# Kernel optimization log

Hardware: AMD Instinct MI355X
Metric: run time of the kernel (lower is better)

## Reference

```python
import jax, jax.numpy as jnp
import numpy as np

H = 16  # heads

def setup_inputs() -> dict:
    key = jax.random.key(0)
    k1, k2, k3 = jax.random.split(key, 3)
    B, N, D = 2, 2048, 1024
    x = jax.random.normal(k1, (B, N, D), dtype=jnp.float32)
    W1 = jax.random.normal(k2, (D, 3 * D), dtype=jnp.float32) * (1.0 / np.sqrt(D))
    b1 = jnp.zeros((3 * D,), dtype=jnp.float32)
    W2 = jax.random.normal(k3, (D, D), dtype=jnp.float32) * (1.0 / np.sqrt(D))
    b2 = jnp.zeros((D,), dtype=jnp.float32)
    return {"x": x, "W1": W1, "b1": b1, "W2": W2, "b2": b2}

def reference(x, W1, b1, W2, b2):
    B, N, D = x.shape
    Dh = D // H  # head dim
    qkv = x @ W1 + b1                         # [B,N,3D]
    q, k, v = jnp.split(qkv, 3, axis=-1)
    q = q.reshape(B, N, H, Dh).transpose(0, 2, 1, 3)  # [B,H,N,Dh]
    k = k.reshape(B, N, H, Dh).transpose(0, 2, 1, 3)
    v = v.reshape(B, N, H, Dh).transpose(0, 2, 1, 3)
    scale = 1.0 / np.sqrt(Dh)
    w = jnp.einsum('bhnd,bhmd->bhnm', q, k) * scale   # [B,H,N,N]
    w = jax.nn.softmax(w, axis=-1)
    out = jnp.einsum('bhnm,bhmd->bhnd', w, v)         # [B,H,N,Dh]
    out = out.transpose(0, 2, 1, 3).reshape(B, N, D)
    return out @ W2 + b2
```

## Files before the change

kernel.cpp:

```cpp
#include <hip/hip_runtime.h>
#include <hip/hip_bf16.h>
#include <stdint.h>

#define B_   2
#define H_   16
#define N_   2048
#define D_   1024
#define DH   64
#define MTOK 4096

#define LOG2E 1.44269504088896f

typedef __attribute__((ext_vector_type(8)))  short bf16x8;
typedef __attribute__((ext_vector_type(4)))  float f32x4;
typedef __attribute__((ext_vector_type(16))) float f32x16;
typedef __attribute__((ext_vector_type(2)))  unsigned u32x2;
typedef __attribute__((ext_vector_type(4)))  unsigned short us4;

#define VMCNT_ASM(N) asm volatile("s_waitcnt vmcnt(" #N ")" ::: "memory")

static __device__ __forceinline__ unsigned short f2bf(float f) {
    union { float f; unsigned u; } v; v.f = f;
    unsigned r = v.u + 0x7fffu + ((v.u >> 16) & 1u);
    return (unsigned short)(r >> 16);
}

static __device__ __forceinline__ unsigned f2u(float x) {
    union { float f; unsigned u; } v; v.f = x; return v.u;
}
static __device__ __forceinline__ float u2f(unsigned x) {
    union { unsigned u; float f; } v; v.u = x; return v.f;
}

static __device__ __forceinline__ unsigned cvt_pk_bf16(float lo, float hi) {
    unsigned r;
    asm("v_cvt_pk_bf16_f32 %0, %1, %2" : "=v"(r) : "v"(lo), "v"(hi));
    return r;
}

static __device__ __forceinline__ bf16x8 frag_from_u32(unsigned a, unsigned b, unsigned c, unsigned d) {
    union { unsigned u[4]; bf16x8 v; } x;
    x.u[0] = a; x.u[1] = b; x.u[2] = c; x.u[3] = d;
    return x.v;
}

static __device__ __forceinline__ void load_lds16(const void* g, void* l) {
    __builtin_amdgcn_global_load_lds(
        (const __attribute__((address_space(1))) unsigned int*)g,
        (__attribute__((address_space(3))) unsigned int*)l, 16, 0, 0);
}

__global__ __launch_bounds__(256) void k_pre(const float* __restrict__ x,
                                             unsigned short* __restrict__ xb,
                                             const float* __restrict__ W1,
                                             unsigned short* __restrict__ w1t,
                                             const float* __restrict__ W2,
                                             unsigned short* __restrict__ w2t) {
    int blk = blockIdx.x;
    int t = threadIdx.x;
    if (blk < 4096) {
        int idx = (blk * 256 + t) * 4;
        float4 v = *(const float4*)(x + idx);
        us4 o;
        o.x = f2bf(v.x); o.y = f2bf(v.y); o.z = f2bf(v.z); o.w = f2bf(v.w);
        *(us4*)(xb + idx) = o;
        return;
    }
    const float* in;
    unsigned short* out;
    int C, bx, by;
    if (blk < 4864) { in = W1; out = w1t; C = 3072; int b2 = blk - 4096; bx = b2 % 48; by = b2 / 48; }
    else            { in = W2; out = w2t; C = 1024; int b2 = blk - 4864; bx = b2 % 16; by = b2 / 16; }
    const int R = 1024;
    __shared__ float tile[64][65];
    int c0 = bx * 64, r0 = by * 64;
    int tr = t >> 4, tc = (t & 15) * 4;
#pragma unroll
    for (int p = 0; p < 4; p++) {
        int row = p * 16 + tr;
        float4 v = *(const float4*)(in + (size_t)(r0 + row) * C + c0 + tc);
        tile[row][tc + 0] = v.x; tile[row][tc + 1] = v.y;
        tile[row][tc + 2] = v.z; tile[row][tc + 3] = v.w;
    }
    __syncthreads();
    int oc = t >> 4, orr = (t & 15) * 4;
#pragma unroll
    for (int p = 0; p < 4; p++) {
        int crow = p * 16 + oc;
        us4 o;
        o.x = f2bf(tile[orr + 0][crow]);
        o.y = f2bf(tile[orr + 1][crow]);
        o.z = f2bf(tile[orr + 2][crow]);
        o.w = f2bf(tile[orr + 3][crow]);
        *(us4*)(out + (size_t)(c0 + crow) * R + r0 + orr) = o;
    }
}

__global__ __launch_bounds__(512, 2) void k_gemm0(const unsigned short* __restrict__ A,
                                                  const unsigned short* __restrict__ Bt,
                                                  const float* __restrict__ bias,
                                                  unsigned short* __restrict__ qdst,
                                                  unsigned short* __restrict__ kdst,
                                                  unsigned short* __restrict__ vdst) {
    __shared__ unsigned short lds[57344];
    const int K = 1024, NT = 16;
    int tid = threadIdx.x;
    int lane = tid & 63, wv = tid >> 6;
    int wm = wv >> 2, wn = wv & 3;
    int F = blockIdx.x;
    int L = (F & 7) * 32 + (F >> 3);
    int n0 = (L % 16) * 192;
    int m0 = (L / 16) * 256;

    f32x4 acc[8][3];
#pragma unroll
    for (int i = 0; i < 8; i++)
#pragma unroll
        for (int j = 0; j < 3; j++) {
            f32x4 z; z[0] = 0.f; z[1] = 0.f; z[2] = 0.f; z[3] = 0.f;
            acc[i][j] = z;
        }

    auto stage = [&](int t) {
        int p = t & 1;
        int k0 = t * 64;
        unsigned short* ab = &lds[p * 16384];
        unsigned short* bb = &lds[32768 + p * 12288];
#pragma unroll
        for (int i = 0; i < 4; i++) {
            int u = i * 512 + tid;
            int r = u >> 3, c8 = u & 7;
            int c8s = c8 ^ (r & 7);
            int db = (i * 512 + wv * 64) * 8;
            load_lds16(A + (size_t)(m0 + r) * K + k0 + c8s * 8, &ab[db]);
            if (i < 3)
                load_lds16(Bt + (size_t)(n0 + r) * K + k0 + c8s * 8, &bb[db]);
        }
    };

    stage(0);
    stage(1);

    const int ml = lane & 15, ul = lane >> 4;
    bf16x8 afr[4], bfr[3];

#pragma unroll 1
    for (int t = 0; t < NT; ++t) {
        if (t < NT - 1) { VMCNT_ASM(7); }
        else            { VMCNT_ASM(0); }
        __builtin_amdgcn_s_barrier();

        const unsigned short* ab = &lds[(t & 1) * 16384];
        const unsigned short* bb = &lds[32768 + (t & 1) * 12288];

#pragma unroll
        for (int kk = 0; kk < 2; ++kk) {
            int ck = ((kk * 4 + ul) ^ (ml & 7)) * 8;
#pragma unroll
            for (int mh = 0; mh < 2; ++mh) {
                if (mh == 0) {
#pragma unroll
                    for (int nj = 0; nj < 3; nj++)
                        bfr[nj] = *(const bf16x8*)&bb[(wn * 48 + nj * 16 + ml) * 64 + ck];
                }
#pragma unroll
                for (int q = 0; q < 4; q++)
                    afr[q] = *(const bf16x8*)&ab[(wm * 128 + (mh * 4 + q) * 16 + ml) * 64 + ck];
                __builtin_amdgcn_s_barrier();
                __builtin_amdgcn_s_setprio(1);
#pragma unroll
                for (int q = 0; q < 4; q++)
#pragma unroll
                    for (int nj = 0; nj < 3; nj++)
                        acc[mh * 4 + q][nj] = __builtin_amdgcn_mfma_f32_16x16x32_bf16(
                            afr[q], bfr[nj], acc[mh * 4 + q][nj], 0, 0, 0);
                __builtin_amdgcn_s_setprio(0);
                __builtin_amdgcn_s_barrier();
            }
        }
        if (t + 2 < NT) stage(t + 2);
    }

#pragma unroll
    for (int nj = 0; nj < 3; nj++) {
        int col = n0 + wn * 48 + nj * 16 + (lane & 15);
        float bv = bias[col];
        int which = col >> 10;
        int hd = (col >> 6) & 15;
        int dh = col & 63;
        float scl = (which == 0) ? (0.125f * LOG2E) : 1.0f;
#pragma unroll
        for (int mi = 0; mi < 8; mi++) {
            int rbase = m0 + wm * 128 + mi * 16 + (lane >> 4) * 4;
#pragma unroll
            for (int r = 0; r < 4; r++) {
                int tok = rbase + r;
                int bb2 = tok >> 11, nn = tok & 2047;
                float vvv = (acc[mi][nj][r] + bv) * scl;
                size_t chunk = ((size_t)(bb2 * H_ + hd) * 64 + (nn >> 5)) * 2048;
                if (which == 0) {
                    qdst[((size_t)(bb2 * H_ + hd) * N_ + nn) * DH + dh] = f2bf(vvv);
                } else if (which == 1) {
                    int lane2 = ((dh >> 3) & 1) * 32 + (nn & 31);
                    kdst[chunk + (dh >> 4) * 512 + lane2 * 8 + (dh & 7)] = f2bf(vvv);
                } else {
                    int lane2 = ((nn >> 3) & 1) * 32 + (dh & 31);
                    int islot = (dh >> 5) * 2 + ((nn >> 4) & 1);
                    vdst[chunk + islot * 512 + lane2 * 8 + (nn & 7)] = f2bf(vvv);
                }
            }
        }
    }
}

__global__ __launch_bounds__(256) void k_gemm1(const unsigned short* __restrict__ A,
                                               const unsigned short* __restrict__ Bt,
                                               const float* __restrict__ bias,
                                               float* __restrict__ outp) {
    __shared__ unsigned short As[3][128 * 32];
    __shared__ unsigned short Bs[3][128 * 32];
    const int K = 1024;
    const int NT = 32;
    int tid = threadIdx.x;
    int lane = tid & 63, wv = tid >> 6;
    int wm = wv >> 1, wn = wv & 1;

    const int NX = 8, CPX = 32;
    int F = blockIdx.x;
    int L = (F & 7) * CPX + (F >> 3);
    int n0 = (L % NX) * 128;
    int m0 = (L / NX) * 128;
    int bIdx = m0 >> 11;
    int ntok0 = m0 & 2047;

    f32x4 acc[4][4];
#pragma unroll
    for (int i = 0; i < 4; i++)
#pragma unroll
        for (int j = 0; j < 4; j++) {
            f32x4 z; z[0] = 0.f; z[1] = 0.f; z[2] = 0.f; z[3] = 0.f;
            acc[i][j] = z;
        }

    auto stage = [&](int buf, int tt) {
        int k0 = tt * 32;
        int hh = k0 >> 6;
        const unsigned short* aptr = A + ((size_t)(bIdx * H_ + hh) * N_ + ntok0) * DH + (k0 & 63);
        const unsigned short* bptr = Bt + (size_t)n0 * K + k0;
#pragma unroll
        for (int i = 0; i < 2; i++) {
            int cidb = i * 256 + wv * 64;
            int cid = cidb + lane;
            int row = cid >> 2;
            int cg  = (cid & 3) ^ (row & 3);
            load_lds16(aptr + (size_t)row * DH + cg * 8, &As[buf][cidb * 8]);
            load_lds16(bptr + (size_t)row * K  + cg * 8, &Bs[buf][cidb * 8]);
        }
    };

    stage(0, 0);
    stage(1, 1);

    const int swz = ((lane >> 4) ^ (lane & 3)) * 8;
    const int ar0 = (wm * 64 + (lane & 15)) * 32 + swz;
    const int br0 = (wn * 64 + (lane & 15)) * 32 + swz;

#pragma unroll 1
    for (int t = 0; t < NT; ++t) {
        int cur = t % 3;
        if (t <= NT - 3) stage((t + 2) % 3, t + 2);
        if (t <= NT - 3)      { VMCNT_ASM(8); }
        else if (t == NT - 2) { VMCNT_ASM(4); }
        else                  { VMCNT_ASM(0); }
        __builtin_amdgcn_s_barrier();
        __builtin_amdgcn_sched_barrier(0);

        bf16x8 af[4], bfr[4];
#pragma unroll
        for (int mi = 0; mi < 4; mi++)
            af[mi] = *(const bf16x8*)&As[cur][ar0 + mi * 16 * 32];
#pragma unroll
        for (int ni = 0; ni < 4; ni++)
            bfr[ni] = *(const bf16x8*)&Bs[cur][br0 + ni * 16 * 32];
#pragma unroll
        for (int mi = 0; mi < 4; mi++)
#pragma unroll
            for (int ni = 0; ni < 4; ni++)
                acc[mi][ni] = __builtin_amdgcn_mfma_f32_16x16x32_bf16(
                    af[mi], bfr[ni], acc[mi][ni], 0, 0, 0);

        __builtin_amdgcn_s_barrier();
    }

#pragma unroll
    for (int ni = 0; ni < 4; ni++) {
        int col = n0 + wn * 64 + ni * 16 + (lane & 15);
        float bv = bias[col];
#pragma unroll
        for (int mi = 0; mi < 4; mi++) {
            int rbase = m0 + wm * 64 + mi * 16 + (lane >> 4) * 4;
#pragma unroll
            for (int r = 0; r < 4; r++)
                outp[(size_t)(rbase + r) * D_ + col] = acc[mi][ni][r] + bv;
        }
    }
}

__global__ __launch_bounds__(512, 2) void k_attn(const unsigned short* __restrict__ qh,
                                                 const unsigned short* __restrict__ ks,
                                                 const unsigned short* __restrict__ vs,
                                                 unsigned short* __restrict__ o) {
    __shared__ unsigned short smem[32768];
    unsigned short* kb = smem;
    unsigned short* vb = smem + 16384;
    float* red = (float*)smem;

    int tid = threadIdx.x;
    int lane = tid & 63, wv = tid >> 6;
    int qsub = wv >> 1;
    int kvh  = wv & 1;
    int F = blockIdx.x;
    int L = (F & 7) * 64 + (F >> 3);
    int bh = L >> 4;
    int q0 = (L & 15) * 128 + qsub * 32;
    int ln = lane & 31, hi = lane >> 5;
    const size_t bhO = (size_t)bh * N_ * DH;

    const unsigned short* qp = qh + bhO;
    bf16x8 qf[4];
#pragma unroll
    for (int kk = 0; kk < 4; kk++)
        qf[kk] = *(const bf16x8*)(qp + (size_t)(q0 + ln) * DH + kk * 16 + hi * 8);

    const unsigned short* kg = ks + (size_t)bh * 131072;
    const unsigned short* vg = vs + (size_t)bh * 131072;

    int sbuf = wv >> 1;
    int sl   = wv & 1;
    int sh   = sbuf & 1;
    unsigned short* dstb = ((sbuf >> 1) ? vb : kb) + sh * 8192 + sl * 2048;
    const unsigned short* srcb = ((sbuf >> 1) ? vg : kg) + (size_t)sh * 65536 + sl * 2048;
    auto stageT = [&](int ring, int t) {
#pragma unroll
        for (int i = 0; i < 4; i++)
            load_lds16(srcb + (size_t)t * 4096 + i * 512 + lane * 8,
                       dstb + ring * 4096 + i * 512);
    };

    f32x16 o0, o1;
#pragma unroll
    for (int r = 0; r < 16; r++) { o0[r] = 0.f; o1[r] = 0.f; }
    float m = -INFINITY, l = 0.f;

    stageT(0, 0);
    __syncthreads();

#pragma unroll 1
    for (int t = 0; t < 16; ++t) {
        int b = t & 1;
        if (t < 15) stageT(b ^ 1, t + 1);

        const unsigned short* kB = kb + kvh * 8192 + b * 4096;
        const unsigned short* vB = vb + kvh * 8192 + b * 4096;

        bf16x8 kfa[4], kfb[4];
#pragma unroll
        for (int i = 0; i < 4; i++) {
            kfa[i] = *(const bf16x8*)&kB[i * 512 + lane * 8];
            kfb[i] = *(const bf16x8*)&kB[2048 + i * 512 + lane * 8];
        }
        f32x16 sa, sb;
#pragma unroll
        for (int r = 0; r < 16; r++) { sa[r] = 0.f; sb[r] = 0.f; }
        __builtin_amdgcn_s_setprio(1);
#pragma unroll
        for (int i = 0; i < 4; i++)
            sa = __builtin_amdgcn_mfma_f32_32x32x16_bf16(kfa[i], qf[i], sa, 0, 0, 0);
#pragma unroll
        for (int i = 0; i < 4; i++)
            sb = __builtin_amdgcn_mfma_f32_32x32x16_bf16(kfb[i], qf[i], sb, 0, 0, 0);
        __builtin_amdgcn_s_setprio(0);

        float mx[8];
#pragma unroll
        for (int i = 0; i < 8; i++)
            mx[i] = fmaxf(fmaxf(sa[i], sa[i + 8]), fmaxf(sb[i], sb[i + 8]));
#pragma unroll
        for (int i = 0; i < 4; i++) mx[i] = fmaxf(mx[i], mx[i + 4]);
        float mt = fmaxf(fmaxf(mx[0], mx[2]), fmaxf(mx[1], mx[3]));
        {
            u32x2 sw = __builtin_amdgcn_permlane32_swap(f2u(mt), f2u(mt), false, false);
            mt = fmaxf(u2f(sw[0]), u2f(sw[1]));
        }
        if (!__all(mt <= m + 8.0f)) {
            float mn = fmaxf(m, mt);
            float fs = __builtin_amdgcn_exp2f(m - mn);
            m = mn;
            l *= fs;
#pragma unroll
            for (int r = 0; r < 16; r++) { o0[r] *= fs; o1[r] *= fs; }
        }
        float pa[16], pb[16];
#pragma unroll
        for (int r = 0; r < 16; r++) {
            pa[r] = __builtin_amdgcn_exp2f(sa[r] - m);
            pb[r] = __builtin_amdgcn_exp2f(sb[r] - m);
        }
        float sm[8];
#pragma unroll
        for (int i = 0; i < 8; i++) sm[i] = (pa[i] + pa[i + 8]) + (pb[i] + pb[i + 8]);
#pragma unroll
        for (int i = 0; i < 4; i++) sm[i] = sm[i] + sm[i + 4];
        float sum = (sm[0] + sm[2]) + (sm[1] + sm[3]);
        {
            u32x2 sw = __builtin_amdgcn_permlane32_swap(f2u(sum), f2u(sum), false, false);
            sum = u2f(sw[0]) + u2f(sw[1]);
        }
        l += sum;

        unsigned pka[8], pkb[8];
#pragma unroll
        for (int i = 0; i < 8; i++) {
            pka[i] = cvt_pk_bf16(pa[2 * i], pa[2 * i + 1]);
            pkb[i] = cvt_pk_bf16(pb[2 * i], pb[2 * i + 1]);
        }
        u32x2 s0 = __builtin_amdgcn_permlane32_swap(pka[0], pka[2], false, false);
        u32x2 s1 = __builtin_amdgcn_permlane32_swap(pka[1], pka[3], false, false);
        u32x2 s2 = __builtin_amdgcn_permlane32_swap(pka[4], pka[6], false, false);
        u32x2 s3 = __builtin_amdgcn_permlane32_swap(pka[5], pka[7], false, false);
        bf16x8 pf0 = frag_from_u32(s0[0], s1[0], s0[1], s1[1]);
        bf16x8 pf1 = frag_from_u32(s2[0], s3[0], s2[1], s3[1]);
        s0 = __builtin_amdgcn_permlane32_swap(pkb[0], pkb[2], false, false);
        s1 = __builtin_amdgcn_permlane32_swap(pkb[1], pkb[3], false, false);
        s2 = __builtin_amdgcn_permlane32_swap(pkb[4], pkb[6], false, false);
        s3 = __builtin_amdgcn_permlane32_swap(pkb[5], pkb[7], false, false);
        bf16x8 pf2 = frag_from_u32(s0[0], s1[0], s0[1], s1[1]);
        bf16x8 pf3 = frag_from_u32(s2[0], s3[0], s2[1], s3[1]);

        bf16x8 vf0, vf1, vf2, vf3;
        vf0 = *(const bf16x8*)&vB[0 * 512 + lane * 8];
        vf1 = *(const bf16x8*)&vB[1 * 512 + lane * 8];
        vf2 = *(const bf16x8*)&vB[2048 + 0 * 512 + lane * 8];
        vf3 = *(const bf16x8*)&vB[2048 + 1 * 512 + lane * 8];
        __builtin_amdgcn_s_setprio(1);
        o0 = __builtin_amdgcn_mfma_f32_32x32x16_bf16(vf0, pf0, o0, 0, 0, 0);
        o0 = __builtin_amdgcn_mfma_f32_32x32x16_bf16(vf1, pf1, o0, 0, 0, 0);
        o0 = __builtin_amdgcn_mfma_f32_32x32x16_bf16(vf2, pf2, o0, 0, 0, 0);
        o0 = __builtin_amdgcn_mfma_f32_32x32x16_bf16(vf3, pf3, o0, 0, 0, 0);
        __builtin_amdgcn_s_setprio(0);
        vf0 = *(const bf16x8*)&vB[2 * 512 + lane * 8];
        vf1 = *(const bf16x8*)&vB[3 * 512 + lane * 8];
        vf2 = *(const bf16x8*)&vB[2048 + 2 * 512 + lane * 8];
        vf3 = *(const bf16x8*)&vB[2048 + 3 * 512 + lane * 8];
        __builtin_amdgcn_s_setprio(1);
        o1 = __builtin_amdgcn_mfma_f32_32x32x16_bf16(vf0, pf0, o1, 0, 0, 0);
        o1 = __builtin_amdgcn_mfma_f32_32x32x16_bf16(vf1, pf1, o1, 0, 0, 0);
        o1 = __builtin_amdgcn_mfma_f32_32x32x16_bf16(vf2, pf2, o1, 0, 0, 0);
        o1 = __builtin_amdgcn_mfma_f32_32x32x16_bf16(vf3, pf3, o1, 0, 0, 0);
        __builtin_amdgcn_s_setprio(0);

        __syncthreads();
    }

    if (kvh == 1) {
        float* rp = red + (qsub * 64 + lane) * 34;
#pragma unroll
        for (int r = 0; r < 16; r++) { rp[r] = o0[r]; rp[16 + r] = o1[r]; }
        rp[32] = m;
        rp[33] = l;
    }
    __syncthreads();
    if (kvh == 0) {
        const float* rp = red + (qsub * 64 + lane) * 34;
        float mb = rp[32], lb = rp[33];
        float mn = fmaxf(m, mb);
        float fa = __builtin_amdgcn_exp2f(m - mn);
        float fb = __builtin_amdgcn_exp2f(mb - mn);
        float inv = 1.0f / (l * fa + lb * fb);
        float ga = fa * inv, gb = fb * inv;
        unsigned short* ob = o + bhO + (size_t)(q0 + ln) * DH;
#pragma unroll
        for (int t2 = 0; t2 < 2; t2++) {
#pragma unroll
            for (int g = 0; g < 4; g++) {
                int d = t2 * 32 + g * 8 + hi * 4;
                int rb = g * 4;
                float a0 = (t2 ? o1[rb + 0] : o0[rb + 0]) * ga + rp[t2 * 16 + rb + 0] * gb;
                float a1 = (t2 ? o1[rb + 1] : o0[rb + 1]) * ga + rp[t2 * 16 + rb + 1] * gb;
                float a2 = (t2 ? o1[rb + 2] : o0[rb + 2]) * ga + rp[t2 * 16 + rb + 2] * gb;
                float a3 = (t2 ? o1[rb + 3] : o0[rb + 3]) * ga + rp[t2 * 16 + rb + 3] * gb;
                us4 w;
                w.x = f2bf(a0); w.y = f2bf(a1); w.z = f2bf(a2); w.w = f2bf(a3);
                *(us4*)(ob + d) = w;
            }
        }
    }
}

extern "C" void kernel_launch(void* const* d_in, const int* in_sizes, int n_in,
                              void* d_out, int out_size, void* d_ws, size_t ws_size,
                              hipStream_t stream) {
    const float* x  = (const float*)d_in[0];
    const float* W1 = (const float*)d_in[1];
    const float* b1 = (const float*)d_in[2];
    const float* W2 = (const float*)d_in[3];
    const float* b2 = (const float*)d_in[4];
    float* out = (float*)d_out;

    char* ws = (char*)d_ws;
    unsigned short* xb   = (unsigned short*)(ws);
    unsigned short* w1t  = (unsigned short*)(ws + 8388608);
    unsigned short* w2t  = (unsigned short*)(ws + 14680064);
    unsigned short* qh   = (unsigned short*)(ws + 16777216);
    unsigned short* ks   = (unsigned short*)(ws + 25165824);
    unsigned short* vsb  = (unsigned short*)(ws + 33554432);
    unsigned short* attn = (unsigned short*)(ws + 41943040);

    k_pre<<<5120, 256, 0, stream>>>(x, xb, W1, w1t, W2, w2t);
    k_gemm0<<<256, 512, 0, stream>>>(xb, w1t, b1, qh, ks, vsb);
    k_attn<<<512, 512, 0, stream>>>(qh, ks, vsb, attn);
    k_gemm1<<<256, 256, 0, stream>>>(attn, w2t, b2, out);
}
```

Measured before the change: 119.9 us.

## Software-pipeline attention QK^T with previous tile softmax-PV and retile output GEMM

The attention loop is restructured so the QK^T MFMAs for tile t are issued in the same iteration as the softmax and PV of tile t-1. V gets a triple-buffered LDS ring, which grows LDS from 64KB to 80KB. This is meant to overlap softmax VALU work with matrix work, at the cost of more LDS per block and possibly lower occupancy. Separately, the output-projection GEMM moves to 512 threads per block with K-steps of 64 and a double-buffered, XOR-swizzled LDS layout, issuing the next stage after compute instead of keeping a triple-buffer ring.

Result: faster. 110.2 us (-8.1%).

```diff
diff --git a/kernel.cpp b/kernel.cpp
--- a/kernel.cpp
+++ b/kernel.cpp
@@ -213,95 +213,96 @@
     }
 }
 
-__global__ __launch_bounds__(256) void k_gemm1(const unsigned short* __restrict__ A,
-                                               const unsigned short* __restrict__ Bt,
-                                               const float* __restrict__ bias,
-                                               float* __restrict__ outp) {
-    __shared__ unsigned short As[3][128 * 32];
-    __shared__ unsigned short Bs[3][128 * 32];
-    const int K = 1024;
-    const int NT = 32;
+__global__ __launch_bounds__(512, 2) void k_gemm1(const unsigned short* __restrict__ A,
+                                                  const unsigned short* __restrict__ Bt,
+                                                  const float* __restrict__ bias,
+                                                  float* __restrict__ outp) {
+    __shared__ unsigned short lds1[32768];
+    const int K = 1024, NT = 16;
     int tid = threadIdx.x;
     int lane = tid & 63, wv = tid >> 6;
-    int wm = wv >> 1, wn = wv & 1;
-
-    const int NX = 8, CPX = 32;
+    int wm = wv >> 2, wn = wv & 3;
     int F = blockIdx.x;
-    int L = (F & 7) * CPX + (F >> 3);
-    int n0 = (L % NX) * 128;
-    int m0 = (L / NX) * 128;
+    int L = (F & 7) * 32 + (F >> 3);
+    int n0 = (L % 8) * 128;
+    int m0 = (L / 8) * 128;
     int bIdx = m0 >> 11;
     int ntok0 = m0 & 2047;
 
-    f32x4 acc[4][4];
+    f32x4 acc[4][2];
 #pragma unroll
     for (int i = 0; i < 4; i++)
 #pragma unroll
-        for (int j = 0; j < 4; j++) {
+        for (int j = 0; j < 2; j++) {
             f32x4 z; z[0] = 0.f; z[1] = 0.f; z[2] = 0.f; z[3] = 0.f;
             acc[i][j] = z;
         }
 
-    auto stage = [&](int buf, int tt) {
-        int k0 = tt * 32;
-        int hh = k0 >> 6;
-        const unsigned short* aptr = A + ((size_t)(bIdx * H_ + hh) * N_ + ntok0) * DH + (k0 & 63);
-        const unsigned short* bptr = Bt + (size_t)n0 * K + k0;
+    auto stage = [&](int t) {
+        int p = t & 1;
+        const unsigned short* aptr = A + ((size_t)(bIdx * H_ + t) * N_ + ntok0) * DH;
+        const unsigned short* bptr = Bt + (size_t)n0 * K + t * 64;
+        unsigned short* ab = &lds1[p * 8192];
+        unsigned short* bb = &lds1[16384 + p * 8192];
 #pragma unroll
         for (int i = 0; i < 2; i++) {
-            int cidb = i * 256 + wv * 64;
-            int cid = cidb + lane;
-            int row = cid >> 2;
-            int cg  = (cid & 3) ^ (row & 3);
-            load_lds16(aptr + (size_t)row * DH + cg * 8, &As[buf][cidb * 8]);
-            load_lds16(bptr + (size_t)row * K  + cg * 8, &Bs[buf][cidb * 8]);
+            int u = i * 512 + tid;
+            int r = u >> 3, c8 = u & 7;
+            int c8s = c8 ^ (r & 7);
+            int db = (i * 512 + wv * 64) * 8;
+            load_lds16(aptr + (size_t)r * DH + c8s * 8, &ab[db]);
+            load_lds16(bptr + (size_t)r * K  + c8s * 8, &bb[db]);
         }
     };
 
-    stage(0, 0);
-    stage(1, 1);
-
-    const int swz = ((lane >> 4) ^ (lane & 3)) * 8;
-    const int ar0 = (wm * 64 + (lane & 15)) * 32 + swz;
-    const int br0 = (wn * 64 + (lane & 15)) * 32 + swz;
+    stage(0);
+    stage(1);
+
+    const int ml = lane & 15, ul = lane >> 4;
+    bf16x8 afr[4], bfr[2];
 
 #pragma unroll 1
     for (int t = 0; t < NT; ++t) {
-        int cur = t % 3;
-        if (t <= NT - 3) stage((t + 2) % 3, t + 2);
-        if (t <= NT - 3)      { VMCNT_ASM(8); }
-        else if (t == NT - 2) { VMCNT_ASM(4); }
-        else                  { VMCNT_ASM(0); }
+        if (t < NT - 1) { VMCNT_ASM(4); }
+        else            { VMCNT_ASM(0); }
         __builtin_amdgcn_s_barrier();
-        __builtin_amdgcn_sched_barrier(0);
-
-        bf16x8 af[4], bfr[4];
-#pragma unroll
-        for (int mi = 0; mi < 4; mi++)
-            af[mi] = *(const bf16x8*)&As[cur][ar0 + mi * 16 * 32];
-#pragma unroll
-        for (int ni = 0; ni < 4; ni++)
-            bfr[ni] = *(const bf16x8*)&Bs[cur][br0 + ni * 16 * 32];
-#pragma unroll
-        for (int mi = 0; mi < 4; mi++)
-#pragma unroll
-            for (int ni = 0; ni < 4; ni++)
-                acc[mi][ni] = __builtin_amdgcn_mfma_f32_16x16x32_bf16(
-                    af[mi], bfr[ni], acc[mi][ni], 0, 0, 0);
-
-        __builtin_amdgcn_s_barrier();
-    }
-
-#pragma unroll
-    for (int ni = 0; ni < 4; ni++) {
-        int col = n0 + wn * 64 + ni * 16 + (lane & 15);
+
+        const unsigned short* ab = &lds1[(t & 1) * 8192];
+        const unsigned short* bb = &lds1[16384 + (t & 1) * 8192];
+
+#pragma unroll
+        for (int kk = 0; kk < 2; ++kk) {
+            int ck = ((kk * 4 + ul) ^ (ml & 7)) * 8;
+#pragma unroll
+            for (int nj = 0; nj < 2; nj++)
+                bfr[nj] = *(const bf16x8*)&bb[(wn * 32 + nj * 16 + ml) * 64 + ck];
+#pragma unroll
+            for (int q = 0; q < 4; q++)
+                afr[q] = *(const bf16x8*)&ab[(wm * 64 + q * 16 + ml) * 64 + ck];
+            __builtin_amdgcn_s_barrier();
+            __builtin_amdgcn_s_setprio(1);
+#pragma unroll
+            for (int q = 0; q < 4; q++)
+#pragma unroll
+                for (int nj = 0; nj < 2; nj++)
+                    acc[q][nj] = __builtin_amdgcn_mfma_f32_16x16x32_bf16(
+                        afr[q], bfr[nj], acc[q][nj], 0, 0, 0);
+            __builtin_amdgcn_s_setprio(0);
+            __builtin_amdgcn_s_barrier();
+        }
+        if (t + 2 < NT) stage(t + 2);
+    }
+
+#pragma unroll
+    for (int nj = 0; nj < 2; nj++) {
+        int col = n0 + wn * 32 + nj * 16 + ml;
         float bv = bias[col];
 #pragma unroll
         for (int mi = 0; mi < 4; mi++) {
             int rbase = m0 + wm * 64 + mi * 16 + (lane >> 4) * 4;
 #pragma unroll
             for (int r = 0; r < 4; r++)
-                outp[(size_t)(rbase + r) * D_ + col] = acc[mi][ni][r] + bv;
+                outp[(size_t)(rbase + r) * D_ + col] = acc[mi][nj][r] + bv;
         }
     }
 }
@@ -310,7 +311,7 @@
                                                  const unsigned short* __restrict__ ks,
                                                  const unsigned short* __restrict__ vs,
                                                  unsigned short* __restrict__ o) {
-    __shared__ unsigned short smem[32768];
+    __shared__ unsigned short smem[40960];
     unsigned short* kb = smem;
     unsigned short* vb = smem + 16384;
     float* red = (float*)smem;
@@ -338,13 +339,14 @@
     int sbuf = wv >> 1;
     int sl   = wv & 1;
     int sh   = sbuf & 1;
-    unsigned short* dstb = ((sbuf >> 1) ? vb : kb) + sh * 8192 + sl * 2048;
     const unsigned short* srcb = ((sbuf >> 1) ? vg : kg) + (size_t)sh * 65536 + sl * 2048;
-    auto stageT = [&](int ring, int t) {
+    auto stageT = [&](int kr, int vr, int t) {
+        unsigned short* dstb = (sbuf >> 1)
+            ? vb + (vr * 2 + sh) * 4096 + sl * 2048
+            : kb + (kr * 2 + sh) * 4096 + sl * 2048;
 #pragma unroll
         for (int i = 0; i < 4; i++)
-            load_lds16(srcb + (size_t)t * 4096 + i * 512 + lane * 8,
-                       dstb + ring * 4096 + i * 512);
+            load_lds16(srcb + (size_t)t * 4096 + i * 512 + lane * 8, dstb + i * 512);
     };
 
     f32x16 o0, o1;
@@ -352,35 +354,7 @@
     for (int r = 0; r < 16; r++) { o0[r] = 0.f; o1[r] = 0.f; }
     float m = -INFINITY, l = 0.f;
 
-    stageT(0, 0);
-    __syncthreads();
-
-#pragma unroll 1
-    for (int t = 0; t < 16; ++t) {
-        int b = t & 1;
-        if (t < 15) stageT(b ^ 1, t + 1);
-
-        const unsigned short* kB = kb + kvh * 8192 + b * 4096;
-        const unsigned short* vB = vb + kvh * 8192 + b * 4096;
-
-        bf16x8 kfa[4], kfb[4];
-#pragma unroll
-        for (int i = 0; i < 4; i++) {
-            kfa[i] = *(const bf16x8*)&kB[i * 512 + lane * 8];
-            kfb[i] = *(const bf16x8*)&kB[2048 + i * 512 + lane * 8];
-        }
-        f32x16 sa, sb;
-#pragma unroll
-        for (int r = 0; r < 16; r++) { sa[r] = 0.f; sb[r] = 0.f; }
-        __builtin_amdgcn_s_setprio(1);
-#pragma unroll
-        for (int i = 0; i < 4; i++)
-            sa = __builtin_amdgcn_mfma_f32_32x32x16_bf16(kfa[i], qf[i], sa, 0, 0, 0);
-#pragma unroll
-        for (int i = 0; i < 4; i++)
-            sb = __builtin_amdgcn_mfma_f32_32x32x16_bf16(kfb[i], qf[i], sb, 0, 0, 0);
-        __builtin_amdgcn_s_setprio(0);
-
+    auto softmax_pv = [&](const f32x16& sa, const f32x16& sb, const unsigned short* vB) {
         float mx[8];
 #pragma unroll
         for (int i = 0; i < 8; i++)
@@ -442,25 +416,50 @@
         vf1 = *(const bf16x8*)&vB[1 * 512 + lane * 8];
         vf2 = *(const bf16x8*)&vB[2048 + 0 * 512 + lane * 8];
         vf3 = *(const bf16x8*)&vB[2048 + 1 * 512 + lane * 8];
-        __builtin_amdgcn_s_setprio(1);
         o0 = __builtin_amdgcn_mfma_f32_32x32x16_bf16(vf0, pf0, o0, 0, 0, 0);
         o0 = __builtin_amdgcn_mfma_f32_32x32x16_bf16(vf1, pf1, o0, 0, 0, 0);
         o0 = __builtin_amdgcn_mfma_f32_32x32x16_bf16(vf2, pf2, o0, 0, 0, 0);
         o0 = __builtin_amdgcn_mfma_f32_32x32x16_bf16(vf3, pf3, o0, 0, 0, 0);
-        __builtin_amdgcn_s_setprio(0);
         vf0 = *(const bf16x8*)&vB[2 * 512 + lane * 8];
         vf1 = *(const bf16x8*)&vB[3 * 512 + lane * 8];
         vf2 = *(const bf16x8*)&vB[2048 + 2 * 512 + lane * 8];
         vf3 = *(const bf16x8*)&vB[2048 + 3 * 512 + lane * 8];
-        __builtin_amdgcn_s_setprio(1);
         o1 = __builtin_amdgcn_mfma_f32_32x32x16_bf16(vf0, pf0, o1, 0, 0, 0);
         o1 = __builtin_amdgcn_mfma_f32_32x32x16_bf16(vf1, pf1, o1, 0, 0, 0);
         o1 = __builtin_amdgcn_mfma_f32_32x32x16_bf16(vf2, pf2, o1, 0, 0, 0);
         o1 = __builtin_amdgcn_mfma_f32_32x32x16_bf16(vf3, pf3, o1, 0, 0, 0);
-        __builtin_amdgcn_s_setprio(0);
+    };
+
+    stageT(0, 0, 0);
+    __syncthreads();
+
+    f32x16 sa, sb;
+#pragma unroll 1
+    for (int t = 0; t < 16; ++t) {
+        if (t < 15) stageT((t + 1) & 1, (t + 1) % 3, t + 1);
+
+        if (t > 0) softmax_pv(sa, sb, vb + (((t - 1) % 3) * 2 + kvh) * 4096);
+
+        const unsigned short* kB = kb + ((t & 1) * 2 + kvh) * 4096;
+        bf16x8 kfa[4], kfb[4];
+#pragma unroll
+        for (int i = 0; i < 4; i++) {
+            kfa[i] = *(const bf16x8*)&kB[i * 512 + lane * 8];
+            kfb[i] = *(const bf16x8*)&kB[2048 + i * 512 + lane * 8];
+        }
+#pragma unroll
+        for (int r = 0; r < 16; r++) { sa[r] = 0.f; sb[r] = 0.f; }
+#pragma unroll
+        for (int i = 0; i < 4; i++)
+            sa = __builtin_amdgcn_mfma_f32_32x32x16_bf16(kfa[i], qf[i], sa, 0, 0, 0);
+#pragma unroll
+        for (int i = 0; i < 4; i++)
+            sb = __builtin_amdgcn_mfma_f32_32x32x16_bf16(kfb[i], qf[i], sb, 0, 0, 0);
 
         __syncthreads();
     }
+    softmax_pv(sa, sb, vb + (0 * 2 + kvh) * 4096);
+    __syncthreads();
 
     if (kvh == 1) {
         float* rp = red + (qsub * 64 + lane) * 34;
@@ -519,5 +518,5 @@
     k_pre<<<5120, 256, 0, stream>>>(x, xb, W1, w1t, W2, w2t);
     k_gemm0<<<256, 512, 0, stream>>>(xb, w1t, b1, qh, ks, vsb);
     k_attn<<<512, 512, 0, stream>>>(qh, ks, vsb, attn);
-    k_gemm1<<<256, 256, 0, stream>>>(attn, w2t, b2, out);
-}
+    k_gemm1<<<256, 512, 0, stream>>>(attn, w2t, b2, out);
+}
```
